# Kernel optimization log

Measured on AMD Instinct MI355X. Metric: run time of the kernel, lower is better.

The kernel has to match this reference:

```python
import jax, jax.numpy as jnp
import numpy as np

LEVELS = [(128, 128), (64, 64), (32, 32), (16, 16)]  # (H, W) per level
B, D, NH, NL, NP, DFF, NLAYERS = 2, 256, 8, 4, 4, 1024, 6
DH = D // NH
Q = sum(h * w for h, w in LEVELS)


def setup_inputs() -> dict:
    key = jax.random.key(0)
    ks = iter(jax.random.split(key, 64))
    inp = {}
    for i, (h, w) in enumerate(LEVELS):
        inp[f"src{i}"] = jax.random.normal(next(ks), (B, D, h, w), jnp.float32)
        inp[f"pos{i}"] = jax.random.normal(next(ks), (B, D, h, w), jnp.float32) * 0.1
    s = 0.02
    def p(shape):
        return jax.random.normal(next(ks), shape, jnp.float32) * s
    inp["level_embed"] = p((NL, D))
    inp["W_off"] = p((NLAYERS, D, NH * NL * NP * 2)); inp["b_off"] = p((NLAYERS, NH * NL * NP * 2))
    inp["W_aw"] = p((NLAYERS, D, NH * NL * NP)); inp["b_aw"] = p((NLAYERS, NH * NL * NP))
    inp["W_v"] = p((NLAYERS, D, D)); inp["b_v"] = p((NLAYERS, D))
    inp["W_out"] = p((NLAYERS, D, D)); inp["b_out"] = p((NLAYERS, D))
    inp["g1"] = jnp.ones((NLAYERS, D)); inp["be1"] = jnp.zeros((NLAYERS, D))
    inp["W1"] = p((NLAYERS, D, DFF)); inp["b1"] = p((NLAYERS, DFF))
    inp["W2"] = p((NLAYERS, DFF, D)); inp["b2"] = p((NLAYERS, D))
    inp["g2"] = jnp.ones((NLAYERS, D)); inp["be2"] = jnp.zeros((NLAYERS, D))
    return inp


def layer_norm(x, g, b, eps=1e-5):
    m = x.mean(-1, keepdims=True)
    v = ((x - m) ** 2).mean(-1, keepdims=True)
    return (x - m) * jax.lax.rsqrt(v + eps) * g + b


def bilinear_sample(v, loc, H, W):
    # v: [B,NH,H*W,DH], loc: [B,NH,Q,NP,2] normalized to [0,1] (grid_sample, align_corners=False, zero pad)
    x = loc[..., 0] * W - 0.5
    y = loc[..., 1] * H - 0.5
    x0f = jnp.floor(x); y0f = jnp.floor(y)
    wx = (x - x0f)[..., None]; wy = (y - y0f)[..., None]
    x0 = x0f.astype(jnp.int32); y0 = y0f.astype(jnp.int32)
    def gather(xi, yi):
        ok = ((xi >= 0) & (xi < W) & (yi >= 0) & (yi < H))[..., None]
        idx = jnp.clip(yi, 0, H - 1) * W + jnp.clip(xi, 0, W - 1)
        b, h, q, pp = idx.shape
        g = jnp.take_along_axis(v, idx.reshape(b, h, q * pp, 1), axis=2).reshape(b, h, q, pp, -1)
        return jnp.where(ok, g, jnp.zeros((), v.dtype))
    v00 = gather(x0, y0); v10 = gather(x0 + 1, y0)
    v01 = gather(x0, y0 + 1); v11 = gather(x0 + 1, y0 + 1)
    return (v00 * (1 - wx) * (1 - wy) + v10 * wx * (1 - wy)
            + v01 * (1 - wx) * wy + v11 * wx * wy)


def deform_attn(x, q, ref, wh, Woff, boff, Waw, baw, Wv, bv, Wout, bout):
    off = (q @ Woff + boff).reshape(B, Q, NH, NL, NP, 2)
    aw = jax.nn.softmax((q @ Waw + baw).reshape(B, Q, NH, NL * NP), -1).reshape(B, Q, NH, NL, NP)
    v = (x @ Wv + bv).reshape(B, Q, NH, DH)
    # sampling locations: [B,Q,NH,NL,NP,2]
    loc = ref[:, :, None, :, None, :] + off / wh[None, None, None, :, None, :]
    out = jnp.zeros((B, Q, NH, DH), x.dtype)
    start = 0
    for lvl, (h, w) in enumerate(LEVELS):
        n = h * w
        vl = v[:, start:start + n].transpose(0, 2, 1, 3)          # [B,NH,n,DH]
        locl = loc[:, :, :, lvl].transpose(0, 2, 1, 3, 4)          # [B,NH,Q,NP,2]
        sampled = bilinear_sample(vl, locl, h, w)                  # [B,NH,Q,NP,DH]
        out = out + jnp.einsum('bqhp,bhqpd->bqhd', aw[:, :, :, lvl], sampled)
        start += n
    return out.reshape(B, Q, D) @ Wout + bout


def _ref_points():
    refs = []
    for h, w in LEVELS:
        ry, rx = jnp.meshgrid(jnp.linspace(0.5, h - 0.5, h) / h,
                              jnp.linspace(0.5, w - 0.5, w) / w, indexing='ij')
        refs.append(jnp.stack([rx.reshape(-1), ry.reshape(-1)], -1))
    r = jnp.concatenate(refs, 0)                                   # [Q,2]
    return jnp.broadcast_to(r[None, :, None, :], (B, Q, NL, 2))    # valid_ratios == 1


def reference(src0, src1, src2, src3, pos0, pos1, pos2, pos3, level_embed,
              W_off, b_off, W_aw, b_aw, W_v, b_v, W_out, b_out,
              g1, be1, W1, b1, W2, b2, g2, be2):
    srcs = [src0, src1, src2, src3]
    poss = [pos0, pos1, pos2, pos3]
    x = jnp.concatenate([s.reshape(B, D, -1).transpose(0, 2, 1) for s in srcs], 1)
    pos = jnp.concatenate([p.reshape(B, D, -1).transpose(0, 2, 1) + level_embed[i][None, None]
                           for i, p in enumerate(poss)], 1)
    ref = _ref_points()
    wh = jnp.array([[w, h] for h, w in LEVELS], jnp.float32)       # offset normalizer (W,H)
    for l in range(NLAYERS):
        q = x + pos
        attn = deform_attn(x, q, ref, wh, W_off[l], b_off[l], W_aw[l], b_aw[l],
                           W_v[l], b_v[l], W_out[l], b_out[l])
        x = layer_norm(x + attn, g1[l], be1[l])
        f = jax.nn.relu(x @ W1[l] + b1[l]) @ W2[l] + b2[l]
        x = layer_norm(x + f, g2[l], be2[l])
    spatial_shapes = jnp.array(LEVELS, jnp.int32)
    sizes = np.array([h * w for h, w in LEVELS])
    level_start_index = jnp.array(np.concatenate([[0], np.cumsum(sizes)[:-1]]), jnp.int32)
    return (x, spatial_shapes, level_start_index)
```

## Files before the change

kernel.cpp:

```cpp
#include <hip/hip_runtime.h>
#include <cstddef>

#define BB 2
#define DD 256
#define NH 8
#define NL 4
#define NP 4
#define DFF 1024
#define NLAYERS 6
#define Q_TOT 21760
#define NTOK (BB * Q_TOT)
#define MTILES (NTOK / 128)
#define LTILES (NTOK / 64)

typedef unsigned short ushort_t;
typedef __attribute__((ext_vector_type(8))) short bh8;
typedef __attribute__((ext_vector_type(4))) float fx4;

__device__ __forceinline__ ushort_t f2b(float x) {
  union { float f; unsigned u; } v; v.f = x;
  unsigned r = v.u + 0x7FFF + ((v.u >> 16) & 1);
  return (ushort_t)(r >> 16);
}
__device__ __forceinline__ float b2f(ushort_t b) {
  union { unsigned u; float f; } v; v.u = ((unsigned)b) << 16; return v.f;
}
__device__ __forceinline__ float b2f_hi(unsigned w) {
  union { unsigned u; float f; } v; v.u = w & 0xFFFF0000u; return v.f;
}
__device__ __forceinline__ float b2f_lo(unsigned w) {
  union { unsigned u; float f; } v; v.u = w << 16; return v.f;
}

__device__ __forceinline__ void gload16(const void* g, void* l) {
  __builtin_amdgcn_global_load_lds(
      (const __attribute__((address_space(1))) unsigned int*)g,
      (__attribute__((address_space(3))) unsigned int*)l, 16, 0, 0);
}

__global__ __launch_bounds__(256) void flatten_level(
    const float* __restrict__ src, const float* __restrict__ pos,
    const float* __restrict__ lemb, float* __restrict__ X,
    ushort_t* __restrict__ Xb, ushort_t* __restrict__ POSb,
    ushort_t* __restrict__ QBb, int HW, int start, int lvl) {
  __shared__ float ts[32][33];
  __shared__ float tp[32][33];
  int p0 = blockIdx.x * 32, d0 = blockIdx.y * 32, b = blockIdx.z;
  const float* sb = src + (size_t)b * DD * HW;
  const float* pb = pos + (size_t)b * DD * HW;
  int px = threadIdx.x;
#pragma unroll
  for (int i = 0; i < 4; ++i) {
    int dl = threadIdx.y + i * 8;
    ts[dl][px] = sb[(size_t)(d0 + dl) * HW + p0 + px];
    tp[dl][px] = pb[(size_t)(d0 + dl) * HW + p0 + px];
  }
  __syncthreads();
  int dx = threadIdx.x;
#pragma unroll
  for (int i = 0; i < 4; ++i) {
    int pl = threadIdx.y + i * 8;
    size_t row = (size_t)b * Q_TOT + start + p0 + pl;
    float s = ts[dx][pl];
    float p = tp[dx][pl] + lemb[lvl * DD + d0 + dx];
    X[row * DD + d0 + dx] = s;
    Xb[row * DD + d0 + dx] = f2b(s);
    POSb[row * DD + d0 + dx] = f2b(p);
    QBb[row * DD + d0 + dx] = f2b(s + p);
  }
}

__global__ __launch_bounds__(256) void transpose_w(const float* __restrict__ W,
                                                   ushort_t* __restrict__ WT,
                                                   int K, int N, int outStride,
                                                   int rowOff) {
  __shared__ float t[32][33];
  int n0 = blockIdx.x * 32, k0 = blockIdx.y * 32, l = blockIdx.z;
  const float* in = W + (size_t)l * K * N;
  ushort_t* out = WT + (size_t)l * outStride;
#pragma unroll
  for (int i = 0; i < 4; ++i) {
    int k = threadIdx.y + i * 8;
    t[k][threadIdx.x] = in[(size_t)(k0 + k) * N + n0 + threadIdx.x];
  }
  __syncthreads();
#pragma unroll
  for (int i = 0; i < 4; ++i) {
    int nn = threadIdx.y + i * 8;
    out[(size_t)(rowOff + n0 + nn) * K + k0 + threadIdx.x] = f2b(t[threadIdx.x][nn]);
  }
}

__global__ void pack_bias(const float* __restrict__ b_off,
                          const float* __restrict__ b_aw,
                          float* __restrict__ b_qa) {
  int l = blockIdx.x, i = threadIdx.x;
  b_qa[l * 384 + i] = (i < 256) ? b_off[l * 256 + i] : b_aw[l * 128 + i - 256];
}

template <int RELU, int OUTBF16>
__global__ __launch_bounds__(256) void gemm_mfma(
    const ushort_t* __restrict__ A, const ushort_t* __restrict__ Bt,
    const float* __restrict__ bias, void* __restrict__ C, int N, int K) {
  __shared__ ushort_t As[128 * 64];
  __shared__ ushort_t Bs[128 * 64];
  int tid = threadIdx.x;
  int m0 = blockIdx.y * 128, n0 = blockIdx.x * 128;
  int wid = tid >> 6, lane = tid & 63;
  int wr = wid >> 1, wc = wid & 1;

  fx4 acc[4][4];
#pragma unroll
  for (int i = 0; i < 4; ++i)
#pragma unroll
    for (int j = 0; j < 4; ++j) acc[i][j] = fx4{0.f, 0.f, 0.f, 0.f};

  const ushort_t* ga = A + (size_t)(m0 + (tid >> 3)) * K + (tid & 7) * 8;
  const ushort_t* gb = Bt + (size_t)(n0 + (tid >> 3)) * K + (tid & 7) * 8;
  int ldsbase = wid * 1024;

  for (int k0 = 0; k0 < K; k0 += 64) {
#pragma unroll
    for (int it = 0; it < 4; ++it) {
      gload16(ga + (size_t)(it * 32) * K + k0, (char*)As + ldsbase + it * 4096);
      gload16(gb + (size_t)(it * 32) * K + k0, (char*)Bs + ldsbase + it * 4096);
    }
    __syncthreads();
#pragma unroll
    for (int kk = 0; kk < 2; ++kk) {
      bh8 af[4], bf[4];
      int cb = kk * 64 + (lane >> 4) * 16;
      int ra = wr * 64 + (lane & 15);
      int rb = wc * 64 + (lane & 15);
#pragma unroll
      for (int i = 0; i < 4; ++i)
        af[i] = *(const bh8*)((const char*)As + (ra + i * 16) * 128 + cb);
#pragma unroll
      for (int i = 0; i < 4; ++i)
        bf[i] = *(const bh8*)((const char*)Bs + (rb + i * 16) * 128 + cb);
#pragma unroll
      for (int i = 0; i < 4; ++i)
#pragma unroll
        for (int j = 0; j < 4; ++j)
          acc[i][j] = __builtin_amdgcn_mfma_f32_16x16x32_bf16(af[i], bf[j], acc[i][j], 0, 0, 0);
    }
    __syncthreads();
  }

  int crow = m0 + wr * 64 + (lane >> 4) * 4;
  int ccol = n0 + wc * 64 + (lane & 15);
#pragma unroll
  for (int j = 0; j < 4; ++j) {
    float bv = bias[ccol + j * 16];
#pragma unroll
    for (int i = 0; i < 4; ++i) {
#pragma unroll
      for (int r = 0; r < 4; ++r) {
        float v = acc[i][j][r] + bv;
        if (RELU) v = fmaxf(v, 0.f);
        size_t idx = (size_t)(crow + i * 16 + r) * N + ccol + j * 16;
        if (OUTBF16) ((ushort_t*)C)[idx] = f2b(v);
        else ((float*)C)[idx] = v;
      }
    }
  }
}

template <int QOUT>
__global__ __launch_bounds__(256) void gemm_ln(
    const ushort_t* __restrict__ A, const ushort_t* __restrict__ Bt,
    const float* __restrict__ bias, const float* __restrict__ gamma,
    const float* __restrict__ beta, float* __restrict__ Xf,
    ushort_t* __restrict__ Xb, const ushort_t* __restrict__ POSb,
    ushort_t* __restrict__ QBb, int K) {
  __shared__ ushort_t As[2][64 * 32];
  __shared__ ushort_t Bs[2][256 * 32];
  __shared__ float red[2][2][64];
  int tid = threadIdx.x;
  int m0 = blockIdx.x * 64;
  int wid = tid >> 6, lane = tid & 63;
  int wr = wid >> 1, wc = wid & 1;

  fx4 acc[2][8];
#pragma unroll
  for (int i = 0; i < 2; ++i)
#pragma unroll
    for (int j = 0; j < 8; ++j) acc[i][j] = fx4{0.f, 0.f, 0.f, 0.f};

  int srow = tid >> 2;
  int sslot = (tid & 3) ^ ((tid >> 3) & 3);
  const ushort_t* ga = A + (size_t)(m0 + srow) * K + sslot * 8;
  const ushort_t* gb = Bt + (size_t)srow * K + sslot * 8;
  int ldsoff = wid * 1024;

  int cbyte = (((lane >> 4) ^ ((lane >> 1) & 3)) << 4);
  int ra = wr * 32 + (lane & 15);
  int rb = wc * 128 + (lane & 15);

  gload16(ga, (char*)As[0] + ldsoff);
#pragma unroll
  for (int it = 0; it < 4; ++it)
    gload16(gb + (size_t)(it * 64) * K, (char*)Bs[0] + it * 4096 + ldsoff);
  __syncthreads();

  int nt = K >> 5;
  int cur = 0;
  for (int t = 0; t < nt; ++t) {
    if (t + 1 < nt) {
      int k1 = (t + 1) << 5;
      gload16(ga + k1, (char*)As[cur ^ 1] + ldsoff);
#pragma unroll
      for (int it = 0; it < 4; ++it)
        gload16(gb + (size_t)(it * 64) * K + k1, (char*)Bs[cur ^ 1] + it * 4096 + ldsoff);
    }
    bh8 af[2], bf[8];
#pragma unroll
    for (int i = 0; i < 2; ++i)
      af[i] = *(const bh8*)((const char*)As[cur] + (ra + i * 16) * 64 + cbyte);
#pragma unroll
    for (int j = 0; j < 8; ++j)
      bf[j] = *(const bh8*)((const char*)Bs[cur] + (rb + j * 16) * 64 + cbyte);
#pragma unroll
    for (int i = 0; i < 2; ++i)
#pragma unroll
      for (int j = 0; j < 8; ++j)
        acc[i][j] = __builtin_amdgcn_mfma_f32_16x16x32_bf16(af[i], bf[j], acc[i][j], 0, 0, 0);
    __syncthreads();
    cur ^= 1;
  }

  int lg = lane >> 4, lc = lane & 15;
  float bv[8], gv[8], bev[8];
#pragma unroll
  for (int j = 0; j < 8; ++j) {
    int col = wc * 128 + j * 16 + lc;
    bv[j] = bias[col];
    gv[j] = gamma[col];
    bev[j] = beta[col];
  }
#pragma unroll
  for (int i = 0; i < 2; ++i) {
#pragma unroll
    for (int r = 0; r < 4; ++r) {
      int rloc = wr * 32 + i * 16 + lg * 4 + r;
      const float* xr = Xf + (size_t)(m0 + rloc) * DD + wc * 128 + lc;
      float s = 0.f, s2 = 0.f;
#pragma unroll
      for (int j = 0; j < 8; ++j) {
        float v = acc[i][j][r] + bv[j] + xr[j * 16];
        acc[i][j][r] = v;
        s += v;
        s2 += v * v;
      }
#pragma unroll
      for (int o = 1; o < 16; o <<= 1) {
        s += __shfl_xor(s, o);
        s2 += __shfl_xor(s2, o);
      }
      if (lc == 0) {
        red[wc][0][rloc] = s;
        red[wc][1][rloc] = s2;
      }
    }
  }
  __syncthreads();
#pragma unroll
  for (int i = 0; i < 2; ++i) {
#pragma unroll
    for (int r = 0; r < 4; ++r) {
      int rloc = wr * 32 + i * 16 + lg * 4 + r;
      float s = red[0][0][rloc] + red[1][0][rloc];
      float s2 = red[0][1][rloc] + red[1][1][rloc];
      float mmean = s * (1.f / 256.f);
      float var = s2 * (1.f / 256.f) - mmean * mmean;
      float inv = rsqrtf(var + 1e-5f);
      size_t rowb = (size_t)(m0 + rloc) * DD + wc * 128 + lc;
#pragma unroll
      for (int j = 0; j < 8; ++j) {
        float y = (acc[i][j][r] - mmean) * inv * gv[j] + bev[j];
        Xf[rowb + j * 16] = y;
        Xb[rowb + j * 16] = f2b(y);
        if (QOUT) QBb[rowb + j * 16] = f2b(y + b2f(POSb[rowb + j * 16]));
      }
    }
  }
}

__global__ __launch_bounds__(256) void sample_v4(const ushort_t* __restrict__ Vb,
                                                 const ushort_t* __restrict__ QA,
                                                 ushort_t* __restrict__ SAMPb) {
  int nb = NTOK / 2;
  int bid = blockIdx.x;
  int newb = (bid & 7) * (nb >> 3) + (bid >> 3);
  int t = newb * 2 + (threadIdx.x >> 7);
  int h = (threadIdx.x >> 4) & 7;
  int p = threadIdx.x & 15;

  int b = (t >= Q_TOT) ? 1 : 0;
  int qi = t - b * Q_TOT;
  int lwq = (qi < 16384) ? 7 : (qi < 20480) ? 6 : (qi < 21504) ? 5 : 4;
  int stq = (qi < 16384) ? 0 : (qi < 20480) ? 16384 : (qi < 21504) ? 20480 : 21504;
  int wt = 1 << lwq;
  int pidx = qi - stq;
  int iy = pidx >> lwq, ix = pidx & (wt - 1);
  float refx = (ix + 0.5f) / (float)wt;
  float refy = (iy + 0.5f) / (float)wt;

  float lgt = b2f(QA[(size_t)t * 384 + 256 + h * 16 + p]);
  float mxv = lgt;
#pragma unroll
  for (int o = 1; o < 16; o <<= 1) mxv = fmaxf(mxv, __shfl_xor(mxv, o, 16));
  float e = __expf(lgt - mxv);
  float sum = e;
#pragma unroll
  for (int o = 1; o < 16; o <<= 1) sum += __shfl_xor(sum, o, 16);
  float a = e / sum;

  int l = p >> 2, pt = p & 3;
  int wl = 128 >> l;
  int LSl = (l > 0 ? 16384 : 0) + (l > 1 ? 4096 : 0) + (l > 2 ? 1024 : 0);
  float fw = (float)wl;
  unsigned ow = *(const unsigned*)(QA + (size_t)t * 384 + h * 32 + l * 8 + pt * 2);
  float ox = b2f_lo(ow), oy = b2f_hi(ow);
  float Xc = refx * fw + ox - 0.5f;
  float Yc = refy * fw + oy - 0.5f;
  float xf = floorf(Xc), yf = floorf(Yc);
  float wx = Xc - xf, wy = Yc - yf;
  int x0 = (int)xf, y0 = (int)yf;
  int x1 = x0 + 1, y1 = y0 + 1;
  float ok_x0 = (x0 >= 0 && x0 < wl) ? 1.f : 0.f;
  float ok_x1 = (x1 >= 0 && x1 < wl) ? 1.f : 0.f;
  float ok_y0 = (y0 >= 0 && y0 < wl) ? 1.f : 0.f;
  float ok_y1 = (y1 >= 0 && y1 < wl) ? 1.f : 0.f;
  int xc0 = min(max(x0, 0), wl - 1), xc1 = min(max(x1, 0), wl - 1);
  int yc0 = min(max(y0, 0), wl - 1), yc1 = min(max(y1, 0), wl - 1);
  float w00 = (1.f - wx) * (1.f - wy) * a * ok_x0 * ok_y0;
  float w10 = wx * (1.f - wy) * a * ok_x1 * ok_y0;
  float w01 = (1.f - wx) * wy * a * ok_x0 * ok_y1;
  float w11 = wx * wy * a * ok_x1 * ok_y1;
  int metaBase = ((b * Q_TOT + LSl + yc0 * wl + xc0) << 8) + h * 32;
  int metaDxy = (int)(((unsigned)((xc1 - xc0) << 8)) |
                      (((unsigned)((yc1 - yc0) * wl) << 8) << 16));
  int metaZ = (int)(((unsigned)f2b(w00) << 16) | f2b(w10));
  int metaW = (int)(((unsigned)f2b(w01) << 16) | f2b(w11));

  int c2 = p * 2;
  float acc0 = 0.f, acc1 = 0.f;
#pragma unroll
  for (int pp = 0; pp < 16; ++pp) {
    int m0v = __shfl(metaBase, pp, 16);
    int m1v = __shfl(metaDxy, pp, 16);
    int mzv = __shfl(metaZ, pp, 16);
    int mwv = __shfl(metaW, pp, 16);
    unsigned dxy = (unsigned)m1v;
    int base = m0v + c2;
    int dx = (int)(dxy & 0xffffu);
    int dy = (int)(dxy >> 16);
    unsigned v00 = *(const unsigned*)(Vb + base);
    unsigned v10 = *(const unsigned*)(Vb + base + dx);
    unsigned v01 = *(const unsigned*)(Vb + base + dy);
    unsigned v11 = *(const unsigned*)(Vb + base + dy + dx);
    unsigned wz = (unsigned)mzv, ww = (unsigned)mwv;
    float f00 = b2f_hi(wz), f10 = b2f_lo(wz);
    float f01 = b2f_hi(ww), f11 = b2f_lo(ww);
    acc0 = fmaf(f00, b2f_lo(v00), acc0);
    acc1 = fmaf(f00, b2f_hi(v00), acc1);
    acc0 = fmaf(f10, b2f_lo(v10), acc0);
    acc1 = fmaf(f10, b2f_hi(v10), acc1);
    acc0 = fmaf(f01, b2f_lo(v01), acc0);
    acc1 = fmaf(f01, b2f_hi(v01), acc1);
    acc0 = fmaf(f11, b2f_lo(v11), acc0);
    acc1 = fmaf(f11, b2f_hi(v11), acc1);
  }
  unsigned outw = (unsigned)f2b(acc0) | ((unsigned)f2b(acc1) << 16);
  *(unsigned*)(SAMPb + (size_t)t * 256 + h * 32 + c2) = outw;
}

__global__ void write_tail(float* __restrict__ t) {
  int i = threadIdx.x;
  float v = 0.f;
  switch (i) {
    case 0: v = 128.f; break;
    case 1: v = 128.f; break;
    case 2: v = 64.f; break;
    case 3: v = 64.f; break;
    case 4: v = 32.f; break;
    case 5: v = 32.f; break;
    case 6: v = 16.f; break;
    case 7: v = 16.f; break;
    case 8: v = 0.f; break;
    case 9: v = 16384.f; break;
    case 10: v = 20480.f; break;
    case 11: v = 21504.f; break;
    default: return;
  }
  t[i] = v;
}

extern "C" void kernel_launch(void* const* d_in, const int* in_sizes, int n_in,
                              void* d_out, int out_size, void* d_ws, size_t ws_size,
                              hipStream_t stream) {
  const float* src[4] = {(const float*)d_in[0], (const float*)d_in[2],
                         (const float*)d_in[4], (const float*)d_in[6]};
  const float* pos[4] = {(const float*)d_in[1], (const float*)d_in[3],
                         (const float*)d_in[5], (const float*)d_in[7]};
  const float* lemb = (const float*)d_in[8];
  const float* W_off = (const float*)d_in[9];
  const float* b_off = (const float*)d_in[10];
  const float* W_aw = (const float*)d_in[11];
  const float* b_aw = (const float*)d_in[12];
  const float* W_v = (const float*)d_in[13];
  const float* b_v = (const float*)d_in[14];
  const float* W_out = (const float*)d_in[15];
  const float* b_out = (const float*)d_in[16];
  const float* g1 = (const float*)d_in[17];
  const float* be1 = (const float*)d_in[18];
  const float* W1 = (const float*)d_in[19];
  const float* b1 = (const float*)d_in[20];
  const float* W2 = (const float*)d_in[21];
  const float* b2 = (const float*)d_in[22];
  const float* g2 = (const float*)d_in[23];
  const float* be2 = (const float*)d_in[24];

  float* X = (float*)d_out;

  char* w = (char*)d_ws;
  const size_t SZ_B = (size_t)NTOK * 256 * 2;
  ushort_t* POSb = (ushort_t*)w;  w += SZ_B;
  ushort_t* Xb = (ushort_t*)w;    w += SZ_B;
  ushort_t* QBb = (ushort_t*)w;   w += SZ_B;
  ushort_t* QAb = (ushort_t*)w;   w += (size_t)NTOK * 384 * 2;
  ushort_t* Vb = (ushort_t*)w;    w += SZ_B;
  ushort_t* SAMPb = (ushort_t*)w; w += SZ_B;
  ushort_t* H1b = (ushort_t*)w;   w += (size_t)NTOK * DFF * 2;
  ushort_t* WT_qa = (ushort_t*)w;  w += (size_t)NLAYERS * 384 * 256 * 2;
  ushort_t* WT_v = (ushort_t*)w;   w += (size_t)NLAYERS * 256 * 256 * 2;
  ushort_t* WT_out = (ushort_t*)w; w += (size_t)NLAYERS * 256 * 256 * 2;
  ushort_t* WT_1 = (ushort_t*)w;   w += (size_t)NLAYERS * 1024 * 256 * 2;
  ushort_t* WT_2 = (ushort_t*)w;   w += (size_t)NLAYERS * 256 * 1024 * 2;
  float* b_qa = (float*)w;         w += (size_t)NLAYERS * 384 * 4;

  transpose_w<<<dim3(8, 8, NLAYERS), dim3(32, 8), 0, stream>>>(W_off, WT_qa, 256, 256, 384 * 256, 0);
  transpose_w<<<dim3(4, 8, NLAYERS), dim3(32, 8), 0, stream>>>(W_aw, WT_qa, 256, 128, 384 * 256, 256);
  pack_bias<<<NLAYERS, 384, 0, stream>>>(b_off, b_aw, b_qa);
  transpose_w<<<dim3(8, 8, NLAYERS), dim3(32, 8), 0, stream>>>(W_v, WT_v, 256, 256, 256 * 256, 0);
  transpose_w<<<dim3(8, 8, NLAYERS), dim3(32, 8), 0, stream>>>(W_out, WT_out, 256, 256, 256 * 256, 0);
  transpose_w<<<dim3(32, 8, NLAYERS), dim3(32, 8), 0, stream>>>(W1, WT_1, 256, 1024, 1024 * 256, 0);
  transpose_w<<<dim3(8, 32, NLAYERS), dim3(32, 8), 0, stream>>>(W2, WT_2, 1024, 256, 256 * 1024, 0);

  static const int LWh[4] = {128, 64, 32, 16};
  static const int LSh[4] = {0, 16384, 20480, 21504};
  for (int l = 0; l < 4; ++l) {
    int hw = LWh[l] * LWh[l];
    dim3 g(hw / 32, DD / 32, BB);
    flatten_level<<<g, dim3(32, 8), 0, stream>>>(src[l], pos[l], lemb, X, Xb, POSb,
                                                 QBb, hw, LSh[l], l);
  }
  write_tail<<<1, 16, 0, stream>>>(X + (size_t)NTOK * DD);

  for (int l = 0; l < NLAYERS; ++l) {
    gemm_mfma<0, 1><<<dim3(3, MTILES), 256, 0, stream>>>(
        QBb, WT_qa + (size_t)l * 384 * 256, b_qa + l * 384, QAb, 384, 256);
    gemm_mfma<0, 1><<<dim3(2, MTILES), 256, 0, stream>>>(
        Xb, WT_v + (size_t)l * 256 * 256, b_v + l * 256, Vb, 256, 256);
    sample_v4<<<NTOK / 2, 256, 0, stream>>>(Vb, QAb, SAMPb);
    gemm_ln<0><<<LTILES, 256, 0, stream>>>(
        SAMPb, WT_out + (size_t)l * 256 * 256, b_out + l * 256,
        g1 + l * DD, be1 + l * DD, X, Xb, POSb, QBb, 256);
    gemm_mfma<1, 1><<<dim3(8, MTILES), 256, 0, stream>>>(
        Xb, WT_1 + (size_t)l * 1024 * 256, b1 + l * DFF, H1b, 1024, 256);
    gemm_ln<1><<<LTILES, 256, 0, stream>>>(
        H1b, WT_2 + (size_t)l * 256 * 1024, b2 + l * 256,
        g2 + l * DD, be2 + l * DD, X, Xb, POSb, QBb, 1024);
  }
}
```

Before: 1.920 ms.

## Triple-buffer gemm_ln K loop with explicit vmcnt waits and barriers

Moves the fused GEMM+LayerNorm kernel from double to triple buffering of its A/B LDS tiles, so two tiles of global-to-LDS loads are in flight. The generic __syncthreads is replaced by explicit s_waitcnt vmcnt counts, raw s_barrier and sched_barrier fences. Fragments are read into registers before a second barrier, which lets the next stage overwrite the buffer while the MFMAs run. The aim is to hide global load latency better, at the cost of 50% more LDS (lower occupancy) and hand-tuned wait counts that depend on each thread issuing exactly five loads per stage.

Measured after the change: 1.951 ms. Within noise of the previous version (+1.6%).

```diff
diff --git a/kernel.cpp b/kernel.cpp
--- a/kernel.cpp
+++ b/kernel.cpp
@@ -173,8 +173,8 @@
     const float* __restrict__ beta, float* __restrict__ Xf,
     ushort_t* __restrict__ Xb, const ushort_t* __restrict__ POSb,
     ushort_t* __restrict__ QBb, int K) {
-  __shared__ ushort_t As[2][64 * 32];
-  __shared__ ushort_t Bs[2][256 * 32];
+  __shared__ ushort_t As[3][64 * 32];
+  __shared__ ushort_t Bs[3][256 * 32];
   __shared__ float red[2][2][64];
   int tid = threadIdx.x;
   int m0 = blockIdx.x * 64;
@@ -197,22 +197,32 @@
   int ra = wr * 32 + (lane & 15);
   int rb = wc * 128 + (lane & 15);
 
-  gload16(ga, (char*)As[0] + ldsoff);
-#pragma unroll
-  for (int it = 0; it < 4; ++it)
-    gload16(gb + (size_t)(it * 64) * K, (char*)Bs[0] + it * 4096 + ldsoff);
-  __syncthreads();
+  auto stage = [&](int buf, int kt) {
+    int kk = kt << 5;
+    gload16(ga + kk, (char*)As[buf] + ldsoff);
+#pragma unroll
+    for (int it = 0; it < 4; ++it)
+      gload16(gb + (size_t)(it * 64) * K + kk, (char*)Bs[buf] + it * 4096 + ldsoff);
+  };
 
   int nt = K >> 5;
+  stage(0, 0);
+  stage(1, 1);
+
   int cur = 0;
   for (int t = 0; t < nt; ++t) {
-    if (t + 1 < nt) {
-      int k1 = (t + 1) << 5;
-      gload16(ga + k1, (char*)As[cur ^ 1] + ldsoff);
-#pragma unroll
-      for (int it = 0; it < 4; ++it)
-        gload16(gb + (size_t)(it * 64) * K + k1, (char*)Bs[cur ^ 1] + it * 4096 + ldsoff);
-    }
+    if (t + 2 < nt) {
+      stage((cur + 2) % 3, t + 2);
+      asm volatile("s_waitcnt vmcnt(10)");
+    } else if (t + 1 < nt) {
+      asm volatile("s_waitcnt vmcnt(5)");
+    } else {
+      asm volatile("s_waitcnt vmcnt(0)");
+    }
+    __builtin_amdgcn_sched_barrier(0);
+    __builtin_amdgcn_s_barrier();
+    __builtin_amdgcn_sched_barrier(0);
+
     bh8 af[2], bf[8];
 #pragma unroll
     for (int i = 0; i < 2; ++i)
@@ -220,13 +230,19 @@
 #pragma unroll
     for (int j = 0; j < 8; ++j)
       bf[j] = *(const bh8*)((const char*)Bs[cur] + (rb + j * 16) * 64 + cbyte);
+    __builtin_amdgcn_sched_barrier(0);
+    asm volatile("s_waitcnt lgkmcnt(0)");
+    __builtin_amdgcn_sched_barrier(0);
+    __builtin_amdgcn_s_barrier();
+    __builtin_amdgcn_sched_barrier(0);
+
 #pragma unroll
     for (int i = 0; i < 2; ++i)
 #pragma unroll
       for (int j = 0; j < 8; ++j)
         acc[i][j] = __builtin_amdgcn_mfma_f32_16x16x32_bf16(af[i], bf[j], acc[i][j], 0, 0, 0);
-    __syncthreads();
-    cur ^= 1;
+
+    cur = (cur + 1) % 3;
   }
 
   int lg = lane >> 4, lc = lane & 15;
```

## Fuse FFN up and down projections with LayerNorm, keeping hidden activations in LDS

Applied to the files above, without the earlier changes.

Replaces the separate FFN1 GEMM, the H1 buffer and the FFN2+LayerNorm kernel with one kernel per 64-row tile. The ReLU hidden tile (64x1024 bf16) is kept in swizzled LDS, and the second GEMM, residual add, LayerNorm and Q=x+pos output are done in the same kernel. The residual stream is also switched to bf16 only, with fp32 written only in the last layer, which cuts global traffic at some accuracy cost. The fused kernel loads MFMA operands straight from global with no double buffering and uses 128KB of LDS, so occupancy and latency hiding may suffer.

Result: faster. 1.846 ms (-3.9%).

```diff
diff --git a/kernel.cpp b/kernel.cpp
--- a/kernel.cpp
+++ b/kernel.cpp
@@ -166,13 +166,10 @@
   }
 }
 
-template <int QOUT>
 __global__ __launch_bounds__(256) void gemm_ln(
     const ushort_t* __restrict__ A, const ushort_t* __restrict__ Bt,
     const float* __restrict__ bias, const float* __restrict__ gamma,
-    const float* __restrict__ beta, float* __restrict__ Xf,
-    ushort_t* __restrict__ Xb, const ushort_t* __restrict__ POSb,
-    ushort_t* __restrict__ QBb, int K) {
+    const float* __restrict__ beta, ushort_t* __restrict__ Xbio, int K) {
   __shared__ ushort_t As[2][64 * 32];
   __shared__ ushort_t Bs[2][256 * 32];
   __shared__ float red[2][2][64];
@@ -243,11 +240,11 @@
 #pragma unroll
     for (int r = 0; r < 4; ++r) {
       int rloc = wr * 32 + i * 16 + lg * 4 + r;
-      const float* xr = Xf + (size_t)(m0 + rloc) * DD + wc * 128 + lc;
+      const ushort_t* xr = Xbio + (size_t)(m0 + rloc) * DD + wc * 128 + lc;
       float s = 0.f, s2 = 0.f;
 #pragma unroll
       for (int j = 0; j < 8; ++j) {
-        float v = acc[i][j][r] + bv[j] + xr[j * 16];
+        float v = acc[i][j][r] + bv[j] + b2f(xr[j * 16]);
         acc[i][j][r] = v;
         s += v;
         s2 += v * v;
@@ -278,9 +275,155 @@
 #pragma unroll
       for (int j = 0; j < 8; ++j) {
         float y = (acc[i][j][r] - mmean) * inv * gv[j] + bev[j];
-        Xf[rowb + j * 16] = y;
-        Xb[rowb + j * 16] = f2b(y);
-        if (QOUT) QBb[rowb + j * 16] = f2b(y + b2f(POSb[rowb + j * 16]));
+        Xbio[rowb + j * 16] = f2b(y);
+      }
+    }
+  }
+}
+
+template <int LAST>
+__global__ __launch_bounds__(512, 2) void ffn_fused(
+    const ushort_t* __restrict__ Xio, const ushort_t* __restrict__ W1t,
+    const float* __restrict__ b1v, const ushort_t* __restrict__ W2t,
+    const float* __restrict__ b2v, const float* __restrict__ gamma,
+    const float* __restrict__ beta, const ushort_t* __restrict__ POSb,
+    ushort_t* __restrict__ QBb, float* __restrict__ Xf) {
+  extern __shared__ char lds[];
+  int tid = threadIdx.x;
+  int w = tid >> 6, l = tid & 63;
+  int l15 = l & 15, l4 = l >> 4, l7 = l & 7;
+  int m0 = blockIdx.x * 64;
+
+  fx4 acc[4][8];
+#pragma unroll
+  for (int i = 0; i < 4; ++i)
+#pragma unroll
+    for (int j = 0; j < 8; ++j) acc[i][j] = fx4{0.f, 0.f, 0.f, 0.f};
+
+  const ushort_t* xb = Xio + (size_t)m0 * 256;
+#pragma unroll
+  for (int kk = 0; kk < 8; ++kk) {
+    bh8 af[4], bf[8];
+#pragma unroll
+    for (int i = 0; i < 4; ++i)
+      af[i] = *(const bh8*)(xb + (size_t)(l15 + 16 * i) * 256 + kk * 32 + l4 * 8);
+#pragma unroll
+    for (int j = 0; j < 8; ++j)
+      bf[j] = *(const bh8*)(W1t + (size_t)(w * 128 + j * 16 + l15) * 256 + kk * 32 + l4 * 8);
+#pragma unroll
+    for (int i = 0; i < 4; ++i)
+#pragma unroll
+      for (int j = 0; j < 8; ++j)
+        acc[i][j] = __builtin_amdgcn_mfma_f32_16x16x32_bf16(af[i], bf[j], acc[i][j], 0, 0, 0);
+  }
+#pragma unroll
+  for (int j = 0; j < 8; ++j) {
+    int n = w * 128 + j * 16 + l15;
+    float bb = b1v[n];
+    int slotbase = n >> 3;
+    int nlo = (n & 7) * 2;
+#pragma unroll
+    for (int i = 0; i < 4; ++i) {
+#pragma unroll
+      for (int r = 0; r < 4; ++r) {
+        int m = l4 * 4 + r + 16 * i;
+        float h = fmaxf(acc[i][j][r] + bb, 0.f);
+        *(ushort_t*)(lds + m * 2048 + ((slotbase ^ (m & 7)) << 4) + nlo) = f2b(h);
+      }
+    }
+  }
+  __syncthreads();
+
+  fx4 acc2[4][2];
+#pragma unroll
+  for (int i = 0; i < 4; ++i)
+#pragma unroll
+    for (int j = 0; j < 2; ++j) acc2[i][j] = fx4{0.f, 0.f, 0.f, 0.f};
+
+#pragma unroll 4
+  for (int kt = 0; kt < 32; ++kt) {
+    bh8 af[4], bf[2];
+#pragma unroll
+    for (int i = 0; i < 4; ++i) {
+      int m = l15 + 16 * i;
+      af[i] = *(const bh8*)(lds + m * 2048 + (((kt * 4 + l4) ^ l7) << 4));
+    }
+#pragma unroll
+    for (int j = 0; j < 2; ++j)
+      bf[j] = *(const bh8*)(W2t + (size_t)(w * 32 + j * 16 + l15) * 1024 + kt * 32 + l4 * 8);
+#pragma unroll
+    for (int i = 0; i < 4; ++i)
+#pragma unroll
+      for (int j = 0; j < 2; ++j)
+        acc2[i][j] = __builtin_amdgcn_mfma_f32_16x16x32_bf16(af[i], bf[j], acc2[i][j], 0, 0, 0);
+  }
+  __syncthreads();
+
+  float* red = (float*)lds;
+  float* minv = (float*)(lds + 4096);
+
+  float gv[2], bev[2], bv2[2];
+#pragma unroll
+  for (int j = 0; j < 2; ++j) {
+    int col = w * 32 + j * 16 + l15;
+    gv[j] = gamma[col];
+    bev[j] = beta[col];
+    bv2[j] = b2v[col];
+  }
+#pragma unroll
+  for (int i = 0; i < 4; ++i) {
+#pragma unroll
+    for (int r = 0; r < 4; ++r) {
+      int m = l4 * 4 + r + 16 * i;
+      float s = 0.f, s2 = 0.f;
+#pragma unroll
+      for (int j = 0; j < 2; ++j) {
+        int col = w * 32 + j * 16 + l15;
+        float v = acc2[i][j][r] + bv2[j] + b2f(Xio[(size_t)(m0 + m) * 256 + col]);
+        acc2[i][j][r] = v;
+        s += v;
+        s2 += v * v;
+      }
+#pragma unroll
+      for (int o = 1; o < 16; o <<= 1) {
+        s += __shfl_xor(s, o);
+        s2 += __shfl_xor(s2, o);
+      }
+      if (l15 == 0) {
+        red[w * 64 + m] = s;
+        red[512 + w * 64 + m] = s2;
+      }
+    }
+  }
+  __syncthreads();
+  if (tid < 64) {
+    float s = 0.f, s2 = 0.f;
+#pragma unroll
+    for (int ww = 0; ww < 8; ++ww) {
+      s += red[ww * 64 + tid];
+      s2 += red[512 + ww * 64 + tid];
+    }
+    float mean = s * (1.f / 256.f);
+    float var = s2 * (1.f / 256.f) - mean * mean;
+    minv[tid * 2] = mean;
+    minv[tid * 2 + 1] = rsqrtf(var + 1e-5f);
+  }
+  __syncthreads();
+  ushort_t* XbOut = (ushort_t*)Xio;
+#pragma unroll
+  for (int i = 0; i < 4; ++i) {
+#pragma unroll
+    for (int r = 0; r < 4; ++r) {
+      int m = l4 * 4 + r + 16 * i;
+      float mean = minv[m * 2], inv = minv[m * 2 + 1];
+      size_t rowb = (size_t)(m0 + m) * 256;
+#pragma unroll
+      for (int j = 0; j < 2; ++j) {
+        int col = w * 32 + j * 16 + l15;
+        float y = (acc2[i][j][r] - mean) * inv * gv[j] + bev[j];
+        XbOut[rowb + col] = f2b(y);
+        if (LAST) Xf[rowb + col] = y;
+        else QBb[rowb + col] = f2b(y + b2f(POSb[rowb + col]));
       }
     }
   }
@@ -432,13 +575,17 @@
   ushort_t* QAb = (ushort_t*)w;   w += (size_t)NTOK * 384 * 2;
   ushort_t* Vb = (ushort_t*)w;    w += SZ_B;
   ushort_t* SAMPb = (ushort_t*)w; w += SZ_B;
-  ushort_t* H1b = (ushort_t*)w;   w += (size_t)NTOK * DFF * 2;
   ushort_t* WT_qa = (ushort_t*)w;  w += (size_t)NLAYERS * 384 * 256 * 2;
   ushort_t* WT_v = (ushort_t*)w;   w += (size_t)NLAYERS * 256 * 256 * 2;
   ushort_t* WT_out = (ushort_t*)w; w += (size_t)NLAYERS * 256 * 256 * 2;
   ushort_t* WT_1 = (ushort_t*)w;   w += (size_t)NLAYERS * 1024 * 256 * 2;
   ushort_t* WT_2 = (ushort_t*)w;   w += (size_t)NLAYERS * 256 * 1024 * 2;
   float* b_qa = (float*)w;         w += (size_t)NLAYERS * 384 * 4;
+
+  hipFuncSetAttribute((const void*)ffn_fused<0>,
+                      hipFuncAttributeMaxDynamicSharedMemorySize, 131072);
+  hipFuncSetAttribute((const void*)ffn_fused<1>,
+                      hipFuncAttributeMaxDynamicSharedMemorySize, 131072);
 
   transpose_w<<<dim3(8, 8, NLAYERS), dim3(32, 8), 0, stream>>>(W_off, WT_qa, 256, 256, 384 * 256, 0);
   transpose_w<<<dim3(4, 8, NLAYERS), dim3(32, 8), 0, stream>>>(W_aw, WT_qa, 256, 128, 384 * 256, 256);
@@ -464,13 +611,19 @@
     gemm_mfma<0, 1><<<dim3(2, MTILES), 256, 0, stream>>>(
         Xb, WT_v + (size_t)l * 256 * 256, b_v + l * 256, Vb, 256, 256);
     sample_v4<<<NTOK / 2, 256, 0, stream>>>(Vb, QAb, SAMPb);
-    gemm_ln<0><<<LTILES, 256, 0, stream>>>(
+    gemm_ln<<<LTILES, 256, 0, stream>>>(
         SAMPb, WT_out + (size_t)l * 256 * 256, b_out + l * 256,
-        g1 + l * DD, be1 + l * DD, X, Xb, POSb, QBb, 256);
-    gemm_mfma<1, 1><<<dim3(8, MTILES), 256, 0, stream>>>(
-        Xb, WT_1 + (size_t)l * 1024 * 256, b1 + l * DFF, H1b, 1024, 256);
-    gemm_ln<1><<<LTILES, 256, 0, stream>>>(
-        H1b, WT_2 + (size_t)l * 256 * 1024, b2 + l * 256,
-        g2 + l * DD, be2 + l * DD, X, Xb, POSb, QBb, 1024);
-  }
-}
+        g1 + l * DD, be1 + l * DD, Xb, 256);
+    if (l + 1 < NLAYERS) {
+      ffn_fused<0><<<LTILES, 512, 131072, stream>>>(
+          Xb, WT_1 + (size_t)l * 1024 * 256, b1 + l * DFF,
+          WT_2 + (size_t)l * 256 * 1024, b2 + l * 256,
+          g2 + l * DD, be2 + l * DD, POSb, QBb, X);
+    } else {
+      ffn_fused<1><<<LTILES, 512, 131072, stream>>>(
+          Xb, WT_1 + (size_t)l * 1024 * 256, b1 + l * DFF,
+          WT_2 + (size_t)l * 256 * 1024, b2 + l * 256,
+          g2 + l * DD, be2 + l * DD, POSb, QBb, X);
+    }
+  }
+}
```
